# Kernel optimization log

Measured on AMD Instinct MI355X. Metric: run time of the kernel, lower is better.

The kernel has to match this reference:

```python
import jax, jax.numpy as jnp
import numpy as np

B, V, C = 8192, 512, 16  # batch, num_variables, constraints per variable
N1 = V + 1  # augmented with bias column


def setup_inputs() -> dict:
    key = jax.random.key(0)
    k1, k2, k3 = jax.random.split(key, 3)
    preds = jax.random.normal(k1, (B, V), dtype=jnp.float32)
    # Acyclic structure: variable v's constraints only reference earlier
    # variables (columns < v) plus the bias column (column V).
    cols = jnp.arange(N1)[None, :]              # [1, N1]
    vids = jnp.arange(V)[:, None]               # [V, 1]
    mask = ((cols < vids) | (cols == V)).astype(jnp.float32)[:, None, :]  # [V,1,N1]
    scale = 0.1
    pos_mats = jax.random.normal(k2, (V, C, N1), dtype=jnp.float32) * scale * mask
    neg_mats = jax.random.normal(k3, (V, C, N1), dtype=jnp.float32) * scale * mask
    return {"preds": preds, "pos_mats": pos_mats, "neg_mats": neg_mats}


def reference(preds, pos_mats, neg_mats):
    # Augment preds with a ones column (bias), as in the original __call__.
    b = preds.shape[0]
    p0 = jnp.concatenate([preds, jnp.ones((b, 1), preds.dtype)], axis=1)  # [B, N1]
    var_ids = jnp.arange(pos_mats.shape[0])

    def step(p, xs):
        pm, nm, v = xs  # pm, nm: [C, N1]
        # apply_matrix: (preds * matrix).sum(-1) with max / min reduction over C
        lower = jnp.einsum('bn,cn->bc', p, pm).max(axis=1)  # [B]
        upper = jnp.einsum('bn,cn->bc', p, nm).min(axis=1)  # [B]
        # get_final_x_correction: clamp prediction into [lower, upper]
        corrected = jnp.minimum(jnp.maximum(p[:, v], lower), upper)
        p = p.at[:, v].set(corrected)
        return p, None

    pf, _ = jax.lax.scan(step, p0, (pos_mats, neg_mats, var_ids))
    return pf[:, : preds.shape[1]]
```

## Files before the change

kernel.cpp:

```cpp
#include <hip/hip_runtime.h>

#define BATCH 8192
#define V 512
#define N1 513
#define KCH 16
#define NCHUNKS 32
#define RB 32
#define NT 1024
#define PKS 520
#define SJ 516

typedef __bf16 bf16_t;
typedef bf16_t bf16x8 __attribute__((ext_vector_type(8)));
typedef float f32x4 __attribute__((ext_vector_type(4)));
typedef float f32x2 __attribute__((ext_vector_type(2)));

#define EPP 4194304ull
#define DV_OFF (EPP * 2ull)
#define BV_OFF (DV_OFF + 1048576ull)

__device__ __forceinline__ f32x4 mfma16(bf16x8 a, bf16x8 b, f32x4 c) {
    return __builtin_amdgcn_mfma_f32_16x16x32_bf16(a, b, c, 0, 0, 0);
}

__global__ __launch_bounds__(256)
void repack_all(const float* __restrict__ pos, const float* __restrict__ neg,
                bf16_t* __restrict__ Mhi, float* __restrict__ Dv,
                float* __restrict__ Bv)
{
    const int bx = blockIdx.x;
    if (bx < 496) {
        const int cc  = (bx >> 4) + 1;
        const int kb  = bx & 15;
        const int nkb = (cc + 1) >> 1;
        if (kb >= nkb) return;
        const int klen = 16 * cc;
        const size_t base = 16384ull * (size_t)((cc * cc) / 4) + (size_t)kb * 16384ull;
        for (int e = threadIdx.x; e < 16384; e += 256) {
            const int t = e >> 9, s = (e >> 3) & 63, jj = e & 7;
            const int c = s & 15, q = s >> 4;
            const int v = cc * 16 + (t >> 1);
            const int k = kb * 32 + 8 * q + jj;
            const float* src = (t & 1) ? neg : pos;
            float x = (k < klen) ? src[(size_t)(v * 16 + c) * N1 + k] : 0.0f;
            if (t & 1) x = -x;
            Mhi[base + e] = (bf16_t)x;
        }
    } else {
        const int e = (bx - 496) * 256 + threadIdx.x;
        if (e < 262144) {
            const int cc = e >> 13, vl = (e >> 9) & 15, j = e & 511;
            const int v = cc * 16 + (j >> 5), c = j & 15;
            const float* src = (j & 16) ? neg : pos;
            const float x = src[(size_t)(v * 16 + c) * N1 + cc * 16 + vl];
            Dv[e] = (j & 16) ? -x : x;
        } else {
            const int e2 = e - 262144;
            const int cc = e2 >> 9, j = e2 & 511;
            const int v = cc * 16 + (j >> 5), c = j & 15;
            const float* src = (j & 16) ? neg : pos;
            const float x = src[(size_t)(v * 16 + c) * N1 + V];
            Bv[e2] = (j & 16) ? -x : x;
        }
    }
}

__global__ __launch_bounds__(NT)
void shield_fused(const float* __restrict__ preds,
                  const bf16_t* __restrict__ Mhi,
                  const float* __restrict__ Dv, const float* __restrict__ Bv,
                  float* __restrict__ out)
{
    __shared__ bf16_t Phi[RB * PKS];
    __shared__ float  S[RB * SJ];

    const int tid  = threadIdx.x;
    const int b0   = blockIdx.x * RB;
    const int lane = tid & 63;
    const int w    = tid >> 6;
    const int cq   = lane & 15;
    const int q    = lane >> 4;
    const int rp0  = w * 2;

    {
        const int r = tid >> 5, seg = tid & 31;
        const float* prow = preds + (size_t)(b0 + r) * V + seg * 16;
        #pragma unroll
        for (int k = 0; k < 16; k += 4) {
            const float4 p4 = *(const float4*)(prow + k);
            const int n = seg * 16 + k;
            Phi[r * PKS + n + 0] = (bf16_t)p4.x;
            Phi[r * PKS + n + 1] = (bf16_t)p4.y;
            Phi[r * PKS + n + 2] = (bf16_t)p4.z;
            Phi[r * PKS + n + 3] = (bf16_t)p4.w;
        }
    }

    int tJ[2];
    #pragma unroll
    for (int tt = 0; tt < 2; ++tt) tJ[tt] = ((2 * w + tt) << 4) + cq;
    const int aoff0 = cq * PKS + 8 * q;
    const int aoff1 = (16 + cq) * PKS + 8 * q;

    f32x4 acc[2][2];
    #pragma unroll
    for (int tt = 0; tt < 2; ++tt) {
        const float b = Bv[tJ[tt]];
        acc[0][tt] = f32x4{b, b, b, b};
        acc[1][tt] = f32x4{b, b, b, b};
    }

    #pragma unroll 1
    for (int cc = 0; cc < NCHUNKS; ++cc) {
        const int v0 = cc * 16;
        const int  ccn  = cc + 1;
        const bool hasN = ccn < NCHUNKS;
        const int  nkbN = hasN ? ((ccn + 1) >> 1) : 0;
        const bf16_t* phN = Mhi + 16384ull * (size_t)((ccn * ccn) / 4)
                          + (size_t)lane * 8 + (size_t)(2 * w) * 512;

        #pragma unroll
        for (int tt = 0; tt < 2; ++tt)
            #pragma unroll
            for (int reg = 0; reg < 4; ++reg) {
                S[(4 * q + reg) * SJ + tJ[tt]]      = acc[0][tt][reg];
                S[(16 + 4 * q + reg) * SJ + tJ[tt]] = acc[1][tt][reg];
            }
        __syncthreads();

        f32x2 s2[8];
        {
            const float4 a0 = *(const float4*)(&S[rp0 * SJ + 8 * lane]);
            const float4 a1 = *(const float4*)(&S[rp0 * SJ + 8 * lane + 4]);
            const float4 c0 = *(const float4*)(&S[(rp0 + 1) * SJ + 8 * lane]);
            const float4 c1 = *(const float4*)(&S[(rp0 + 1) * SJ + 8 * lane + 4]);
            s2[0] = f32x2{a0.x, c0.x}; s2[1] = f32x2{a0.y, c0.y};
            s2[2] = f32x2{a0.z, c0.z}; s2[3] = f32x2{a0.w, c0.w};
            s2[4] = f32x2{a1.x, c1.x}; s2[5] = f32x2{a1.y, c1.y};
            s2[6] = f32x2{a1.z, c1.z}; s2[7] = f32x2{a1.w, c1.w};
        }

        if (hasN) {
            #pragma unroll
            for (int tt = 0; tt < 2; ++tt) {
                const float b = Bv[(ccn << 9) + tJ[tt]];
                acc[0][tt] = f32x4{b, b, b, b};
                acc[1][tt] = f32x4{b, b, b, b};
            }
        }

        #pragma unroll
        for (int vl = 0; vl < KCH; ++vl) {
            const int vcur = v0 + vl;
            const bool doKb = hasN && (vl < nkbN - 1);

            bf16x8 fa0, fa1, fb0, fb1;
            if (doKb) {
                const int k0 = vl * 32;
                fa0 = *(const bf16x8*)(Phi + aoff0 + k0);
                fa1 = *(const bf16x8*)(Phi + aoff1 + k0);
                const bf16_t* pb = phN + (size_t)k0 * 512;
                fb0 = *(const bf16x8*)(pb);
                fb1 = *(const bf16x8*)(pb + 512);
            }

            float dv[8], po[2];
            {
                const float* dp = Dv + ((size_t)vcur << 9) + 8 * lane;
                const float4 d0 = *(const float4*)(dp);
                const float4 d1 = *(const float4*)(dp + 4);
                dv[0]=d0.x; dv[1]=d0.y; dv[2]=d0.z; dv[3]=d0.w;
                dv[4]=d1.x; dv[5]=d1.y; dv[6]=d1.z; dv[7]=d1.w;
                po[0] = (float)Phi[rp0 * PKS + vcur];
                po[1] = (float)Phi[(rp0 + 1) * PKS + vcur];
            }

            f32x2 m01 = __builtin_elementwise_max(s2[0], s2[1]);
            f32x2 m23 = __builtin_elementwise_max(s2[2], s2[3]);
            f32x2 m45 = __builtin_elementwise_max(s2[4], s2[5]);
            f32x2 m67 = __builtin_elementwise_max(s2[6], s2[7]);
            f32x2 mx  = __builtin_elementwise_max(
                            __builtin_elementwise_max(m01, m23),
                            __builtin_elementwise_max(m45, m67));
            float red[2];
            #pragma unroll
            for (int r = 0; r < 2; ++r)
                red[r] = fmaxf(mx[r], __shfl_xor(mx[r], 1, 64));
            float pc[2];
            #pragma unroll
            for (int r = 0; r < 2; ++r) {
                const float lw  = __shfl(red[r], 4 * vl, 64);
                const float nup = __shfl(red[r], 4 * vl + 2, 64);
                pc[r] = fminf(fmaxf(po[r], lw), -nup);
            }
            if (lane == 4 * vl) {
                Phi[rp0 * PKS + vcur]       = (bf16_t)pc[0];
                Phi[(rp0 + 1) * PKS + vcur] = (bf16_t)pc[1];
            }
            const f32x2 pcv = {pc[0], pc[1]};
            #pragma unroll
            for (int jj = 0; jj < 8; ++jj) {
                const f32x2 dsp = {dv[jj], dv[jj]};
                s2[jj] = __builtin_elementwise_fma(dsp, pcv, s2[jj]);
            }

            if (doKb) {
                acc[0][0] = mfma16(fa0, fb0, acc[0][0]);
                acc[1][0] = mfma16(fa1, fb0, acc[1][0]);
                acc[0][1] = mfma16(fa0, fb1, acc[0][1]);
                acc[1][1] = mfma16(fa1, fb1, acc[1][1]);
            }
        }

        __syncthreads();

        if (hasN) {
            const int k0 = (nkbN - 1) * 32;
            const bf16x8 fa0 = *(const bf16x8*)(Phi + aoff0 + k0);
            const bf16x8 fa1 = *(const bf16x8*)(Phi + aoff1 + k0);
            const bf16_t* pb = phN + (size_t)k0 * 512;
            const bf16x8 fb0 = *(const bf16x8*)(pb);
            const bf16x8 fb1 = *(const bf16x8*)(pb + 512);
            acc[0][0] = mfma16(fa0, fb0, acc[0][0]);
            acc[1][0] = mfma16(fa1, fb0, acc[1][0]);
            acc[0][1] = mfma16(fa0, fb1, acc[0][1]);
            acc[1][1] = mfma16(fa1, fb1, acc[1][1]);
        }
    }

    {
        const int r = tid >> 5, seg = tid & 31;
        float* orow = out + (size_t)(b0 + r) * V + seg * 16;
        #pragma unroll
        for (int k = 0; k < 16; k += 4) {
            const int n = seg * 16 + k;
            float4 o;
            o.x = (float)Phi[r * PKS + n + 0];
            o.y = (float)Phi[r * PKS + n + 1];
            o.z = (float)Phi[r * PKS + n + 2];
            o.w = (float)Phi[r * PKS + n + 3];
            *(float4*)(orow + k) = o;
        }
    }
}

extern "C" void kernel_launch(void* const* d_in, const int* in_sizes, int n_in,
                              void* d_out, int out_size, void* d_ws, size_t ws_size,
                              hipStream_t stream) {
    const float* preds = (const float*)d_in[0];
    const float* pos   = (const float*)d_in[1];
    const float* neg   = (const float*)d_in[2];
    float* o = (float*)d_out;
    char* base = (char*)d_ws;
    bf16_t* Mhi = (bf16_t*)base;
    float*  Dv  = (float*)(base + DV_OFF);
    float*  Bv  = (float*)(base + BV_OFF);
    repack_all<<<dim3(1584), 256, 0, stream>>>(pos, neg, Mhi, Dv, Bv);
    shield_fused<<<dim3(BATCH / RB), NT, 0, stream>>>(preds, Mhi, Dv, Bv, o);
}
```

Before: 420.2 us.

## Halve variable chunk size to 8 with triangular bf16 matrix packing

Shrinks the sequential chunk from 16 to 8 variables, which doubles the number of chunks to 64. The constraint matrices are repacked into a new triangular layout, and each wave now owns a single 16-column MFMA tile instead of two. The per-variable serial reduction becomes smaller (4 values per lane plus an extra shuffle), and the off-critical-path MFMA work is spread over two k-block slots per step. This is meant to cut the dependent-chain work per variable and the MFMA work wasted on zero padding, at the cost of twice as many block-wide barriers and S-buffer round trips.

```diff
diff --git a/kernel.cpp b/kernel.cpp
--- a/kernel.cpp
+++ b/kernel.cpp
@@ -3,21 +3,21 @@
 #define BATCH 8192
 #define V 512
 #define N1 513
-#define KCH 16
-#define NCHUNKS 32
+#define KCH 8
+#define NCH 64
 #define RB 32
 #define NT 1024
 #define PKS 520
-#define SJ 516
+#define SJ 260
 
 typedef __bf16 bf16_t;
 typedef bf16_t bf16x8 __attribute__((ext_vector_type(8)));
 typedef float f32x4 __attribute__((ext_vector_type(4)));
 typedef float f32x2 __attribute__((ext_vector_type(2)));
 
-#define EPP 4194304ull
-#define DV_OFF (EPP * 2ull)
-#define BV_OFF (DV_OFF + 1048576ull)
+#define MHI_ELEMS 4325376ull
+#define DV_OFF (MHI_ELEMS * 2ull)
+#define BV_OFF (DV_OFF + 524288ull)
 
 __device__ __forceinline__ f32x4 mfma16(bf16x8 a, bf16x8 b, f32x4 c) {
     return __builtin_amdgcn_mfma_f32_16x16x32_bf16(a, b, c, 0, 0, 0);
@@ -29,17 +29,18 @@
                 float* __restrict__ Bv)
 {
     const int bx = blockIdx.x;
-    if (bx < 496) {
+    if (bx < 1008) {
         const int cc  = (bx >> 4) + 1;
         const int kb  = bx & 15;
-        const int nkb = (cc + 1) >> 1;
+        const int nkb = (cc + 3) >> 2;
         if (kb >= nkb) return;
-        const int klen = 16 * cc;
-        const size_t base = 16384ull * (size_t)((cc * cc) / 4) + (size_t)kb * 16384ull;
-        for (int e = threadIdx.x; e < 16384; e += 256) {
-            const int t = e >> 9, s = (e >> 3) & 63, jj = e & 7;
-            const int c = s & 15, q = s >> 4;
-            const int v = cc * 16 + (t >> 1);
+        const int klen = 8 * cc;
+        const int qq = (cc - 1) >> 2, ss = (cc - 1) & 3;
+        const size_t base = ((size_t)(2 * qq * (qq + 1) + ss * (qq + 1)) + kb) * 8192ull;
+        for (int e = threadIdx.x; e < 8192; e += 256) {
+            const int t = e >> 9, s5 = (e >> 3) & 63, jj = e & 7;
+            const int c = s5 & 15, q = s5 >> 4;
+            const int v = cc * 8 + (t >> 1);
             const int k = kb * 32 + 8 * q + jj;
             const float* src = (t & 1) ? neg : pos;
             float x = (k < klen) ? src[(size_t)(v * 16 + c) * N1 + k] : 0.0f;
@@ -47,17 +48,17 @@
             Mhi[base + e] = (bf16_t)x;
         }
     } else {
-        const int e = (bx - 496) * 256 + threadIdx.x;
-        if (e < 262144) {
-            const int cc = e >> 13, vl = (e >> 9) & 15, j = e & 511;
-            const int v = cc * 16 + (j >> 5), c = j & 15;
+        const int e = (bx - 1008) * 256 + threadIdx.x;
+        if (e < 131072) {
+            const int cc = e >> 11, vl = (e >> 8) & 7, j = e & 255;
+            const int v = cc * 8 + (j >> 5), c = j & 15;
             const float* src = (j & 16) ? neg : pos;
-            const float x = src[(size_t)(v * 16 + c) * N1 + cc * 16 + vl];
+            const float x = src[(size_t)(v * 16 + c) * N1 + cc * 8 + vl];
             Dv[e] = (j & 16) ? -x : x;
         } else {
-            const int e2 = e - 262144;
-            const int cc = e2 >> 9, j = e2 & 511;
-            const int v = cc * 16 + (j >> 5), c = j & 15;
+            const int e2 = e - 131072;
+            const int cc = e2 >> 8, j = e2 & 255;
+            const int v = cc * 8 + (j >> 5), c = j & 15;
             const float* src = (j & 16) ? neg : pos;
             const float x = src[(size_t)(v * 16 + c) * N1 + V];
             Bv[e2] = (j & 16) ? -x : x;
@@ -96,119 +97,112 @@
         }
     }
 
-    int tJ[2];
-    #pragma unroll
-    for (int tt = 0; tt < 2; ++tt) tJ[tt] = ((2 * w + tt) << 4) + cq;
+    const int j0    = 16 * w + cq;
     const int aoff0 = cq * PKS + 8 * q;
     const int aoff1 = (16 + cq) * PKS + 8 * q;
 
-    f32x4 acc[2][2];
-    #pragma unroll
-    for (int tt = 0; tt < 2; ++tt) {
-        const float b = Bv[tJ[tt]];
-        acc[0][tt] = f32x4{b, b, b, b};
-        acc[1][tt] = f32x4{b, b, b, b};
+    f32x4 acc[2];
+    {
+        const float b = Bv[j0];
+        acc[0] = f32x4{b, b, b, b};
+        acc[1] = f32x4{b, b, b, b};
     }
 
     #pragma unroll 1
-    for (int cc = 0; cc < NCHUNKS; ++cc) {
-        const int v0 = cc * 16;
+    for (int cc = 0; cc < NCH; ++cc) {
+        const int v0 = cc * 8;
         const int  ccn  = cc + 1;
-        const bool hasN = ccn < NCHUNKS;
-        const int  nkbN = hasN ? ((ccn + 1) >> 1) : 0;
-        const bf16_t* phN = Mhi + 16384ull * (size_t)((ccn * ccn) / 4)
-                          + (size_t)lane * 8 + (size_t)(2 * w) * 512;
-
-        #pragma unroll
-        for (int tt = 0; tt < 2; ++tt)
-            #pragma unroll
-            for (int reg = 0; reg < 4; ++reg) {
-                S[(4 * q + reg) * SJ + tJ[tt]]      = acc[0][tt][reg];
-                S[(16 + 4 * q + reg) * SJ + tJ[tt]] = acc[1][tt][reg];
-            }
+        const bool hasN = ccn < NCH;
+        const int  nkbN = hasN ? ((ccn + 3) >> 2) : 0;
+        const int  qq = (ccn - 1) >> 2, ss = (ccn - 1) & 3;
+        const bf16_t* phN = Mhi + 8192ull * (size_t)(2 * qq * (qq + 1) + ss * (qq + 1))
+                          + (size_t)w * 512 + (size_t)lane * 8;
+
+        #pragma unroll
+        for (int reg = 0; reg < 4; ++reg) {
+            S[(4 * q + reg) * SJ + j0]      = acc[0][reg];
+            S[(16 + 4 * q + reg) * SJ + j0] = acc[1][reg];
+        }
         __syncthreads();
 
-        f32x2 s2[8];
+        f32x2 s2[4];
         {
-            const float4 a0 = *(const float4*)(&S[rp0 * SJ + 8 * lane]);
-            const float4 a1 = *(const float4*)(&S[rp0 * SJ + 8 * lane + 4]);
-            const float4 c0 = *(const float4*)(&S[(rp0 + 1) * SJ + 8 * lane]);
-            const float4 c1 = *(const float4*)(&S[(rp0 + 1) * SJ + 8 * lane + 4]);
+            const float4 a0 = *(const float4*)(&S[rp0 * SJ + 4 * lane]);
+            const float4 c0 = *(const float4*)(&S[(rp0 + 1) * SJ + 4 * lane]);
             s2[0] = f32x2{a0.x, c0.x}; s2[1] = f32x2{a0.y, c0.y};
             s2[2] = f32x2{a0.z, c0.z}; s2[3] = f32x2{a0.w, c0.w};
-            s2[4] = f32x2{a1.x, c1.x}; s2[5] = f32x2{a1.y, c1.y};
-            s2[6] = f32x2{a1.z, c1.z}; s2[7] = f32x2{a1.w, c1.w};
         }
 
         if (hasN) {
-            #pragma unroll
-            for (int tt = 0; tt < 2; ++tt) {
-                const float b = Bv[(ccn << 9) + tJ[tt]];
-                acc[0][tt] = f32x4{b, b, b, b};
-                acc[1][tt] = f32x4{b, b, b, b};
-            }
+            const float b = Bv[(ccn << 8) + j0];
+            acc[0] = f32x4{b, b, b, b};
+            acc[1] = f32x4{b, b, b, b};
         }
 
         #pragma unroll
         for (int vl = 0; vl < KCH; ++vl) {
             const int vcur = v0 + vl;
-            const bool doKb = hasN && (vl < nkbN - 1);
-
-            bf16x8 fa0, fa1, fb0, fb1;
-            if (doKb) {
+            const bool doA = hasN && (vl < nkbN - 1);
+            const bool doB = hasN && (vl + 8 < nkbN - 1);
+
+            bf16x8 faA0, faA1, fbA, faB0, faB1, fbB;
+            if (doA) {
                 const int k0 = vl * 32;
-                fa0 = *(const bf16x8*)(Phi + aoff0 + k0);
-                fa1 = *(const bf16x8*)(Phi + aoff1 + k0);
-                const bf16_t* pb = phN + (size_t)k0 * 512;
-                fb0 = *(const bf16x8*)(pb);
-                fb1 = *(const bf16x8*)(pb + 512);
-            }
-
-            float dv[8], po[2];
+                faA0 = *(const bf16x8*)(Phi + aoff0 + k0);
+                faA1 = *(const bf16x8*)(Phi + aoff1 + k0);
+                fbA  = *(const bf16x8*)(phN + (size_t)vl * 8192);
+            }
+            if (doB) {
+                const int k0 = (vl + 8) * 32;
+                faB0 = *(const bf16x8*)(Phi + aoff0 + k0);
+                faB1 = *(const bf16x8*)(Phi + aoff1 + k0);
+                fbB  = *(const bf16x8*)(phN + (size_t)(vl + 8) * 8192);
+            }
+
+            float dv[4], po[2];
             {
-                const float* dp = Dv + ((size_t)vcur << 9) + 8 * lane;
-                const float4 d0 = *(const float4*)(dp);
-                const float4 d1 = *(const float4*)(dp + 4);
-                dv[0]=d0.x; dv[1]=d0.y; dv[2]=d0.z; dv[3]=d0.w;
-                dv[4]=d1.x; dv[5]=d1.y; dv[6]=d1.z; dv[7]=d1.w;
+                const float4 d0 = *(const float4*)(Dv + ((size_t)vcur << 8) + 4 * lane);
+                dv[0] = d0.x; dv[1] = d0.y; dv[2] = d0.z; dv[3] = d0.w;
                 po[0] = (float)Phi[rp0 * PKS + vcur];
                 po[1] = (float)Phi[(rp0 + 1) * PKS + vcur];
             }
 
-            f32x2 m01 = __builtin_elementwise_max(s2[0], s2[1]);
-            f32x2 m23 = __builtin_elementwise_max(s2[2], s2[3]);
-            f32x2 m45 = __builtin_elementwise_max(s2[4], s2[5]);
-            f32x2 m67 = __builtin_elementwise_max(s2[6], s2[7]);
-            f32x2 mx  = __builtin_elementwise_max(
-                            __builtin_elementwise_max(m01, m23),
-                            __builtin_elementwise_max(m45, m67));
+            const f32x2 mx = __builtin_elementwise_max(
+                                 __builtin_elementwise_max(s2[0], s2[1]),
+                                 __builtin_elementwise_max(s2[2], s2[3]));
             float red[2];
             #pragma unroll
-            for (int r = 0; r < 2; ++r)
-                red[r] = fmaxf(mx[r], __shfl_xor(mx[r], 1, 64));
+            for (int r = 0; r < 2; ++r) {
+                float m = mx[r];
+                m = fmaxf(m, __shfl_xor(m, 1, 64));
+                m = fmaxf(m, __shfl_xor(m, 2, 64));
+                red[r] = m;
+            }
             float pc[2];
             #pragma unroll
             for (int r = 0; r < 2; ++r) {
-                const float lw  = __shfl(red[r], 4 * vl, 64);
-                const float nup = __shfl(red[r], 4 * vl + 2, 64);
+                const float lw  = __shfl(red[r], 8 * vl, 64);
+                const float nup = __shfl(red[r], 8 * vl + 4, 64);
                 pc[r] = fminf(fmaxf(po[r], lw), -nup);
             }
-            if (lane == 4 * vl) {
+            if (lane == 8 * vl) {
                 Phi[rp0 * PKS + vcur]       = (bf16_t)pc[0];
                 Phi[(rp0 + 1) * PKS + vcur] = (bf16_t)pc[1];
             }
             const f32x2 pcv = {pc[0], pc[1]};
             #pragma unroll
-            for (int jj = 0; jj < 8; ++jj) {
+            for (int jj = 0; jj < 4; ++jj) {
                 const f32x2 dsp = {dv[jj], dv[jj]};
                 s2[jj] = __builtin_elementwise_fma(dsp, pcv, s2[jj]);
             }
 
-            if (doKb) {
-                acc[0][0] = mfma16(fa0, fb0, acc[0][0]);
-                acc[1][0] = mfma16(fa1, fb0, acc[1][0]);
-                acc[0][1] = mfma16(fa0, fb1, acc[0][1]);
-                acc[1][1] = mfma16(fa1, fb1, acc[1][1]);
+            if (doA) {
+                acc[0] = mfma16(faA0, fbA, acc[0]);
+                acc[1] = mfma16(faA1, fbA, acc[1]);
+            }
+            if (doB) {
+                acc[0] = mfma16(faB0, fbB, acc[0]);
+                acc[1] = mfma16(faB1, fbB, acc[1]);
             }
         }
 
@@ -218,13 +212,9 @@
             const int k0 = (nkbN - 1) * 32;
             const bf16x8 fa0 = *(const bf16x8*)(Phi + aoff0 + k0);
             const bf16x8 fa1 = *(const bf16x8*)(Phi + aoff1 + k0);
-            const bf16_t* pb = phN + (size_t)k0 * 512;
-            const bf16x8 fb0 = *(const bf16x8*)(pb);
-            const bf16x8 fb1 = *(const bf16x8*)(pb + 512);
-            acc[0][0] = mfma16(fa0, fb0, acc[0][0]);
-            acc[1][0] = mfma16(fa1, fb0, acc[1][0]);
-            acc[0][1] = mfma16(fa0, fb1, acc[0][1]);
-            acc[1][1] = mfma16(fa1, fb1, acc[1][1]);
+            const bf16x8 fb  = *(const bf16x8*)(phN + (size_t)(nkbN - 1) * 8192);
+            acc[0] = mfma16(fa0, fb, acc[0]);
+            acc[1] = mfma16(fa1, fb, acc[1]);
         }
     }
 
```

Result: slower. 450.4 us (+7.2%).

## Replace block barriers with per-wave flag dataflow and per-variable wave ownership

Applied to the files above, without the earlier changes.

Restructures the fused kernel so each of the 16 waves owns one variable per chunk. A wave computes that variable's constraint dot products with MFMA and then applies intra-chunk corrections from earlier waves, which it waits for by spinning on LDS flags instead of block-wide barriers. The repack kernel writes a new per-variable weight layout and transposed diagonal and bias tables to match. The aim is to drop the per-chunk staging through shared memory and the __syncthreads stalls, and to overlap the next chunk's matmul with the serial clamp chain. In exchange it relies on volatile spin-waits with sleep, which can serialize waves (wave 15 waits on all others) and has subtle memory-ordering risks.

```diff
diff --git a/kernel.cpp b/kernel.cpp
--- a/kernel.cpp
+++ b/kernel.cpp
@@ -3,76 +3,83 @@
 #define BATCH 8192
 #define V 512
 #define N1 513
-#define KCH 16
-#define NCHUNKS 32
+#define NCH 32
 #define RB 32
 #define NT 1024
 #define PKS 520
-#define SJ 516
 
 typedef __bf16 bf16_t;
 typedef bf16_t bf16x8 __attribute__((ext_vector_type(8)));
 typedef float f32x4 __attribute__((ext_vector_type(4)));
-typedef float f32x2 __attribute__((ext_vector_type(2)));
-
-#define EPP 4194304ull
-#define DV_OFF (EPP * 2ull)
-#define BV_OFF (DV_OFF + 1048576ull)
+
+#define MB_ELEMS 4194304ull
+#define DVT_OFF  (MB_ELEMS * 2ull)
+#define BT_OFF   (DVT_OFF + 1048576ull)
 
 __device__ __forceinline__ f32x4 mfma16(bf16x8 a, bf16x8 b, f32x4 c) {
     return __builtin_amdgcn_mfma_f32_16x16x32_bf16(a, b, c, 0, 0, 0);
 }
+__device__ __forceinline__ f32x4 shflx4(f32x4 x, int m) {
+    f32x4 r;
+    r[0] = __shfl_xor(x[0], m, 64);
+    r[1] = __shfl_xor(x[1], m, 64);
+    r[2] = __shfl_xor(x[2], m, 64);
+    r[3] = __shfl_xor(x[3], m, 64);
+    return r;
+}
+__device__ __forceinline__ f32x4 splat4(float s) { return f32x4{s, s, s, s}; }
 
 __global__ __launch_bounds__(256)
 void repack_all(const float* __restrict__ pos, const float* __restrict__ neg,
-                bf16_t* __restrict__ Mhi, float* __restrict__ Dv,
-                float* __restrict__ Bv)
+                bf16_t* __restrict__ Mb, float* __restrict__ DvT,
+                float* __restrict__ Bt)
 {
     const int bx = blockIdx.x;
-    if (bx < 496) {
-        const int cc  = (bx >> 4) + 1;
+    if (bx < 7936) {
+        const int v   = 16 + (bx >> 4);
         const int kb  = bx & 15;
+        const int cc  = v >> 4;
         const int nkb = (cc + 1) >> 1;
         if (kb >= nkb) return;
         const int klen = 16 * cc;
-        const size_t base = 16384ull * (size_t)((cc * cc) / 4) + (size_t)kb * 16384ull;
-        for (int e = threadIdx.x; e < 16384; e += 256) {
-            const int t = e >> 9, s = (e >> 3) & 63, jj = e & 7;
+        const size_t vbase = 16384ull * (size_t)((cc * cc) >> 2)
+                           + (size_t)(v & 15) * 1024ull * nkb
+                           + (size_t)kb * 512ull;
+        for (int e = threadIdx.x; e < 1024; e += 256) {
+            const int mat = e >> 9, s = (e >> 3) & 63, jj = e & 7;
             const int c = s & 15, q = s >> 4;
-            const int v = cc * 16 + (t >> 1);
             const int k = kb * 32 + 8 * q + jj;
-            const float* src = (t & 1) ? neg : pos;
+            const float* src = mat ? neg : pos;
             float x = (k < klen) ? src[(size_t)(v * 16 + c) * N1 + k] : 0.0f;
-            if (t & 1) x = -x;
-            Mhi[base + e] = (bf16_t)x;
-        }
+            if (mat) x = -x;
+            Mb[vbase + (size_t)mat * 512ull * nkb + (e & 511)] = (bf16_t)x;
+        }
+    } else if (bx < 8960) {
+        const int e = (bx - 7936) * 256 + threadIdx.x;
+        const int mat = e & 1, c = (e >> 1) & 15, w = (e >> 5) & 15;
+        const int vcol = e >> 9;
+        const int v = (vcol & ~15) + w;
+        const float* src = mat ? neg : pos;
+        const float x = src[(size_t)(v * 16 + c) * N1 + vcol];
+        DvT[e] = mat ? -x : x;
     } else {
-        const int e = (bx - 496) * 256 + threadIdx.x;
-        if (e < 262144) {
-            const int cc = e >> 13, vl = (e >> 9) & 15, j = e & 511;
-            const int v = cc * 16 + (j >> 5), c = j & 15;
-            const float* src = (j & 16) ? neg : pos;
-            const float x = src[(size_t)(v * 16 + c) * N1 + cc * 16 + vl];
-            Dv[e] = (j & 16) ? -x : x;
-        } else {
-            const int e2 = e - 262144;
-            const int cc = e2 >> 9, j = e2 & 511;
-            const int v = cc * 16 + (j >> 5), c = j & 15;
-            const float* src = (j & 16) ? neg : pos;
-            const float x = src[(size_t)(v * 16 + c) * N1 + V];
-            Bv[e2] = (j & 16) ? -x : x;
-        }
+        const int e = (bx - 8960) * 256 + threadIdx.x;
+        const int mat = e & 1, c = (e >> 1) & 15, v = e >> 5;
+        const float* src = mat ? neg : pos;
+        const float x = src[(size_t)(v * 16 + c) * N1 + V];
+        Bt[e] = mat ? -x : x;
     }
 }
 
 __global__ __launch_bounds__(NT)
-void shield_fused(const float* __restrict__ preds,
-                  const bf16_t* __restrict__ Mhi,
-                  const float* __restrict__ Dv, const float* __restrict__ Bv,
+void shield_async(const float* __restrict__ preds,
+                  const bf16_t* __restrict__ Mb,
+                  const float* __restrict__ DvT, const float* __restrict__ Bt,
                   float* __restrict__ out)
 {
     __shared__ bf16_t Phi[RB * PKS];
-    __shared__ float  S[RB * SJ];
+    __shared__ float  Pc[16 * 32];
+    __shared__ int    flags[16];
 
     const int tid  = threadIdx.x;
     const int b0   = blockIdx.x * RB;
@@ -80,7 +87,8 @@
     const int w    = tid >> 6;
     const int cq   = lane & 15;
     const int q    = lane >> 4;
-    const int rp0  = w * 2;
+
+    if (tid < 16) flags[tid] = 0;
 
     {
         const int r = tid >> 5, seg = tid & 31;
@@ -95,138 +103,113 @@
             Phi[r * PKS + n + 3] = (bf16_t)p4.w;
         }
     }
-
-    int tJ[2];
-    #pragma unroll
-    for (int tt = 0; tt < 2; ++tt) tJ[tt] = ((2 * w + tt) << 4) + cq;
+    __syncthreads();
+
     const int aoff0 = cq * PKS + 8 * q;
     const int aoff1 = (16 + cq) * PKS + 8 * q;
+    volatile int* vf = flags;
 
     f32x4 acc[2][2];
-    #pragma unroll
-    for (int tt = 0; tt < 2; ++tt) {
-        const float b = Bv[tJ[tt]];
-        acc[0][tt] = f32x4{b, b, b, b};
-        acc[1][tt] = f32x4{b, b, b, b};
+    {
+        const float2 b2 = *(const float2*)(Bt + ((size_t)w * 16 + cq) * 2);
+        acc[0][0] = splat4(b2.x); acc[1][0] = splat4(b2.x);
+        acc[0][1] = splat4(b2.y); acc[1][1] = splat4(b2.y);
     }
 
     #pragma unroll 1
-    for (int cc = 0; cc < NCHUNKS; ++cc) {
-        const int v0 = cc * 16;
-        const int  ccn  = cc + 1;
-        const bool hasN = ccn < NCHUNKS;
-        const int  nkbN = hasN ? ((ccn + 1) >> 1) : 0;
-        const bf16_t* phN = Mhi + 16384ull * (size_t)((ccn * ccn) / 4)
-                          + (size_t)lane * 8 + (size_t)(2 * w) * 512;
-
+    for (int cc = 0; cc < NCH; ++cc) {
+        const int v0  = cc * 16;
+        const int vme = v0 + w;
+        const int nkb = (cc + 1) >> 1;
+
+        if (cc > 0) {
+            while (vf[15] < cc) __builtin_amdgcn_s_sleep(1);
+            __threadfence_block();
+            const size_t vbase = 16384ull * (size_t)((cc * cc) >> 2)
+                               + (size_t)w * 1024ull * nkb + (size_t)lane * 8;
+            const int k0 = (nkb - 1) * 32;
+            const bf16x8 fa0 = *(const bf16x8*)(Phi + aoff0 + k0);
+            const bf16x8 fa1 = *(const bf16x8*)(Phi + aoff1 + k0);
+            const bf16x8 fb0 = *(const bf16x8*)(Mb + vbase + (size_t)(nkb - 1) * 512);
+            const bf16x8 fb1 = *(const bf16x8*)(Mb + vbase + (size_t)(2 * nkb - 1) * 512);
+            acc[0][0] = mfma16(fa0, fb0, acc[0][0]);
+            acc[1][0] = mfma16(fa1, fb0, acc[1][0]);
+            acc[0][1] = mfma16(fa0, fb1, acc[0][1]);
+            acc[1][1] = mfma16(fa1, fb1, acc[1][1]);
+        }
+
+        #pragma unroll 1
+        for (int vl = 0; vl < w; ++vl) {
+            while (vf[vl] <= cc) __builtin_amdgcn_s_sleep(1);
+            __threadfence_block();
+            const float2 d2 =
+                *(const float2*)(DvT + ((size_t)((v0 + vl) * 16 + w) * 16 + cq) * 2);
+            const f32x4 pc0 = *(const f32x4*)(Pc + vl * 32 + 4 * q);
+            const f32x4 pc1 = *(const f32x4*)(Pc + vl * 32 + 16 + 4 * q);
+            const f32x4 d0s = splat4(d2.x);
+            const f32x4 d1s = splat4(d2.y);
+            acc[0][0] = __builtin_elementwise_fma(d0s, pc0, acc[0][0]);
+            acc[1][0] = __builtin_elementwise_fma(d0s, pc1, acc[1][0]);
+            acc[0][1] = __builtin_elementwise_fma(d1s, pc0, acc[0][1]);
+            acc[1][1] = __builtin_elementwise_fma(d1s, pc1, acc[1][1]);
+        }
+
+        f32x4 r00 = acc[0][0], r10 = acc[1][0], r01 = acc[0][1], r11 = acc[1][1];
         #pragma unroll
-        for (int tt = 0; tt < 2; ++tt)
+        for (int m = 1; m < 16; m <<= 1) {
+            r00 = __builtin_elementwise_max(r00, shflx4(r00, m));
+            r10 = __builtin_elementwise_max(r10, shflx4(r10, m));
+            r01 = __builtin_elementwise_max(r01, shflx4(r01, m));
+            r11 = __builtin_elementwise_max(r11, shflx4(r11, m));
+        }
+
+        if (cq == 0) {
+            f32x4 po0, po1;
             #pragma unroll
             for (int reg = 0; reg < 4; ++reg) {
-                S[(4 * q + reg) * SJ + tJ[tt]]      = acc[0][tt][reg];
-                S[(16 + 4 * q + reg) * SJ + tJ[tt]] = acc[1][tt][reg];
+                po0[reg] = (float)Phi[(4 * q + reg) * PKS + vme];
+                po1[reg] = (float)Phi[(16 + 4 * q + reg) * PKS + vme];
             }
-        __syncthreads();
-
-        f32x2 s2[8];
-        {
-            const float4 a0 = *(const float4*)(&S[rp0 * SJ + 8 * lane]);
-            const float4 a1 = *(const float4*)(&S[rp0 * SJ + 8 * lane + 4]);
-            const float4 c0 = *(const float4*)(&S[(rp0 + 1) * SJ + 8 * lane]);
-            const float4 c1 = *(const float4*)(&S[(rp0 + 1) * SJ + 8 * lane + 4]);
-            s2[0] = f32x2{a0.x, c0.x}; s2[1] = f32x2{a0.y, c0.y};
-            s2[2] = f32x2{a0.z, c0.z}; s2[3] = f32x2{a0.w, c0.w};
-            s2[4] = f32x2{a1.x, c1.x}; s2[5] = f32x2{a1.y, c1.y};
-            s2[6] = f32x2{a1.z, c1.z}; s2[7] = f32x2{a1.w, c1.w};
-        }
-
-        if (hasN) {
+            const f32x4 pc0 = __builtin_elementwise_min(
+                                  __builtin_elementwise_max(po0, r00), -r01);
+            const f32x4 pc1 = __builtin_elementwise_min(
+                                  __builtin_elementwise_max(po1, r10), -r11);
+            *(f32x4*)(Pc + w * 32 + 4 * q)      = pc0;
+            *(f32x4*)(Pc + w * 32 + 16 + 4 * q) = pc1;
             #pragma unroll
-            for (int tt = 0; tt < 2; ++tt) {
-                const float b = Bv[(ccn << 9) + tJ[tt]];
-                acc[0][tt] = f32x4{b, b, b, b};
-                acc[1][tt] = f32x4{b, b, b, b};
+            for (int reg = 0; reg < 4; ++reg) {
+                Phi[(4 * q + reg) * PKS + vme]      = (bf16_t)pc0[reg];
+                Phi[(16 + 4 * q + reg) * PKS + vme] = (bf16_t)pc1[reg];
             }
         }
-
-        #pragma unroll
-        for (int vl = 0; vl < KCH; ++vl) {
-            const int vcur = v0 + vl;
-            const bool doKb = hasN && (vl < nkbN - 1);
-
-            bf16x8 fa0, fa1, fb0, fb1;
-            if (doKb) {
-                const int k0 = vl * 32;
-                fa0 = *(const bf16x8*)(Phi + aoff0 + k0);
-                fa1 = *(const bf16x8*)(Phi + aoff1 + k0);
-                const bf16_t* pb = phN + (size_t)k0 * 512;
-                fb0 = *(const bf16x8*)(pb);
-                fb1 = *(const bf16x8*)(pb + 512);
-            }
-
-            float dv[8], po[2];
-            {
-                const float* dp = Dv + ((size_t)vcur << 9) + 8 * lane;
-                const float4 d0 = *(const float4*)(dp);
-                const float4 d1 = *(const float4*)(dp + 4);
-                dv[0]=d0.x; dv[1]=d0.y; dv[2]=d0.z; dv[3]=d0.w;
-                dv[4]=d1.x; dv[5]=d1.y; dv[6]=d1.z; dv[7]=d1.w;
-                po[0] = (float)Phi[rp0 * PKS + vcur];
-                po[1] = (float)Phi[(rp0 + 1) * PKS + vcur];
-            }
-
-            f32x2 m01 = __builtin_elementwise_max(s2[0], s2[1]);
-            f32x2 m23 = __builtin_elementwise_max(s2[2], s2[3]);
-            f32x2 m45 = __builtin_elementwise_max(s2[4], s2[5]);
-            f32x2 m67 = __builtin_elementwise_max(s2[6], s2[7]);
-            f32x2 mx  = __builtin_elementwise_max(
-                            __builtin_elementwise_max(m01, m23),
-                            __builtin_elementwise_max(m45, m67));
-            float red[2];
-            #pragma unroll
-            for (int r = 0; r < 2; ++r)
-                red[r] = fmaxf(mx[r], __shfl_xor(mx[r], 1, 64));
-            float pc[2];
-            #pragma unroll
-            for (int r = 0; r < 2; ++r) {
-                const float lw  = __shfl(red[r], 4 * vl, 64);
-                const float nup = __shfl(red[r], 4 * vl + 2, 64);
-                pc[r] = fminf(fmaxf(po[r], lw), -nup);
-            }
-            if (lane == 4 * vl) {
-                Phi[rp0 * PKS + vcur]       = (bf16_t)pc[0];
-                Phi[(rp0 + 1) * PKS + vcur] = (bf16_t)pc[1];
-            }
-            const f32x2 pcv = {pc[0], pc[1]};
-            #pragma unroll
-            for (int jj = 0; jj < 8; ++jj) {
-                const f32x2 dsp = {dv[jj], dv[jj]};
-                s2[jj] = __builtin_elementwise_fma(dsp, pcv, s2[jj]);
-            }
-
-            if (doKb) {
+        __threadfence_block();
+        if (lane == 0) flags[w] = cc + 1;
+
+        const int ccn = cc + 1;
+        if (ccn < NCH) {
+            const int nkbN = (ccn + 1) >> 1;
+            const size_t vbN = 16384ull * (size_t)((ccn * ccn) >> 2)
+                             + (size_t)w * 1024ull * nkbN + (size_t)lane * 8;
+            const float2 b2 =
+                *(const float2*)(Bt + ((size_t)(ccn * 16 + w) * 16 + cq) * 2);
+            acc[0][0] = splat4(b2.x); acc[1][0] = splat4(b2.x);
+            acc[0][1] = splat4(b2.y); acc[1][1] = splat4(b2.y);
+            #pragma unroll 1
+            for (int kb = 0; kb < nkbN - 1; ++kb) {
+                const int k0 = kb * 32;
+                const bf16x8 fa0 = *(const bf16x8*)(Phi + aoff0 + k0);
+                const bf16x8 fa1 = *(const bf16x8*)(Phi + aoff1 + k0);
+                const bf16x8 fb0 = *(const bf16x8*)(Mb + vbN + (size_t)kb * 512);
+                const bf16x8 fb1 = *(const bf16x8*)(Mb + vbN + (size_t)(nkbN + kb) * 512);
                 acc[0][0] = mfma16(fa0, fb0, acc[0][0]);
                 acc[1][0] = mfma16(fa1, fb0, acc[1][0]);
                 acc[0][1] = mfma16(fa0, fb1, acc[0][1]);
                 acc[1][1] = mfma16(fa1, fb1, acc[1][1]);
             }
         }
-
-        __syncthreads();
-
-        if (hasN) {
-            const int k0 = (nkbN - 1) * 32;
-            const bf16x8 fa0 = *(const bf16x8*)(Phi + aoff0 + k0);
-            const bf16x8 fa1 = *(const bf16x8*)(Phi + aoff1 + k0);
-            const bf16_t* pb = phN + (size_t)k0 * 512;
-            const bf16x8 fb0 = *(const bf16x8*)(pb);
-            const bf16x8 fb1 = *(const bf16x8*)(pb + 512);
-            acc[0][0] = mfma16(fa0, fb0, acc[0][0]);
-            acc[1][0] = mfma16(fa1, fb0, acc[1][0]);
-            acc[0][1] = mfma16(fa0, fb1, acc[0][1]);
-            acc[1][1] = mfma16(fa1, fb1, acc[1][1]);
-        }
-    }
+    }
+
+    __syncthreads();
 
     {
         const int r = tid >> 5, seg = tid & 31;
@@ -252,9 +235,9 @@
     const float* neg   = (const float*)d_in[2];
     float* o = (float*)d_out;
     char* base = (char*)d_ws;
-    bf16_t* Mhi = (bf16_t*)base;
-    float*  Dv  = (float*)(base + DV_OFF);
-    float*  Bv  = (float*)(base + BV_OFF);
-    repack_all<<<dim3(1584), 256, 0, stream>>>(pos, neg, Mhi, Dv, Bv);
-    shield_fused<<<dim3(BATCH / RB), NT, 0, stream>>>(preds, Mhi, Dv, Bv, o);
-}
+    bf16_t* Mb  = (bf16_t*)base;
+    float*  DvT = (float*)(base + DVT_OFF);
+    float*  Bt  = (float*)(base + BT_OFF);
+    repack_all<<<dim3(9024), 256, 0, stream>>>(pos, neg, Mb, DvT, Bt);
+    shield_async<<<dim3(BATCH / RB), NT, 0, stream>>>(preds, Mb, DvT, Bt, o);
+}
```

New measurement: 765.9 us. 1.82x slower.
